# Performance work log

Hardware: AMD Instinct MI355X
Metric: run time of the kernel (lower is better)

## Reference

```python
import jax, jax.numpy as jnp
import numpy as np

PH, PW = 7, 7          # pooled output size (fixed by offset shape in module)
SPP = 2                # sample_per_part: bilinear samples per bin edge
SS = 0.0625            # spatial_scale = 1/16
TRANS_STD = 0.1


def setup_inputs() -> dict:
    key = jax.random.key(0)
    k1, k2, k3, k4, k5 = jax.random.split(key, 5)
    B, C, H, W = 8, 256, 168, 168
    N = 512
    img = W / SS  # input-image extent = 2688
    features = jax.random.normal(k1, (B, C, H, W), dtype=jnp.float32)
    bidx = jax.random.randint(k2, (N,), 0, B).astype(jnp.float32)
    xs = jnp.sort(jax.random.uniform(k3, (N, 2), minval=0.0, maxval=img - 1.0), axis=1)
    ys = jnp.sort(jax.random.uniform(k4, (N, 2), minval=0.0, maxval=img - 1.0), axis=1)
    rois = jnp.stack([bidx, xs[:, 0], ys[:, 0],
                      jnp.minimum(xs[:, 1] + 16.0, img - 1.0),
                      jnp.minimum(ys[:, 1] + 16.0, img - 1.0)], axis=1)
    offset = jax.random.normal(k5, (N, 2, PH, PW), dtype=jnp.float32)
    return {"features": features, "rois": rois, "offset": offset}


def _deform_roi_pool(features, rois, offset):
    B, C, H, W = features.shape
    off = offset * TRANS_STD  # module scales offsets by trans_std
    bidx = jax.lax.stop_gradient(rois[:, 0]).astype(jnp.int32)
    x1, y1, x2, y2 = rois[:, 1], rois[:, 2], rois[:, 3], rois[:, 4]
    # DCN kernel ROI geometry (0.5-pixel aligned, min size 0.1)
    sw = x1 * SS - 0.5
    sh = y1 * SS - 0.5
    rw = jnp.maximum((x2 + 1.0) * SS - 0.5 - sw, 0.1)
    rh = jnp.maximum((y2 + 1.0) * SS - 0.5 - sh, 0.1)
    bin_w, bin_h = rw / PW, rh / PH
    sub_w, sub_h = bin_w / SPP, bin_h / SPP

    e5 = lambda v: v[:, None, None, None, None]  # [N] -> [N,1,1,1,1]
    pw = jnp.arange(PW, dtype=features.dtype).reshape(1, 1, PW, 1, 1)
    ph = jnp.arange(PH, dtype=features.dtype).reshape(1, PH, 1, 1, 1)
    iw = (jnp.arange(SPP, dtype=features.dtype) + 0.5).reshape(1, 1, 1, 1, SPP)
    ih = (jnp.arange(SPP, dtype=features.dtype) + 0.5).reshape(1, 1, 1, SPP, 1)
    offx = off[:, 0][:, :, :, None, None]  # [N,PH,PW,1,1]
    offy = off[:, 1][:, :, :, None, None]

    # sample coords [N,PH,PW,SPP,SPP]: bin start + per-bin learned shift + sub-sample
    x = e5(sw) + pw * e5(bin_w) + offx * e5(rw) + iw * e5(sub_w)
    y = e5(sh) + ph * e5(bin_h) + offy * e5(rh) + ih * e5(sub_h)

    valid = (x > -0.5) & (x < W - 0.5) & (y > -0.5) & (y < H - 0.5)
    xc = jnp.clip(x, 0.0, W - 1.0)
    yc = jnp.clip(y, 0.0, H - 1.0)
    x0f, y0f = jnp.floor(xc), jnp.floor(yc)
    lx, ly = xc - x0f, yc - y0f
    x0 = x0f.astype(jnp.int32)
    y0 = y0f.astype(jnp.int32)
    x1i = jnp.minimum(x0 + 1, W - 1)
    y1i = jnp.minimum(y0 + 1, H - 1)

    # flat gather over (batch, h, w), channels vectorized
    featf = jnp.transpose(features, (0, 2, 3, 1)).reshape(B * H * W, C)
    base = e5(bidx) * (H * W)
    g = lambda yy, xx: featf[base + yy * W + xx]  # [N,PH,PW,SPP,SPP,C]

    w00 = ((1 - ly) * (1 - lx))[..., None]
    w01 = ((1 - ly) * lx)[..., None]
    w10 = (ly * (1 - lx))[..., None]
    w11 = (ly * lx)[..., None]
    val = w00 * g(y0, x0) + w01 * g(y0, x1i) + w10 * g(y1i, x0) + w11 * g(y1i, x1i)
    val = jnp.where(valid[..., None], val, 0.0)

    s = val.sum(axis=(3, 4))                                   # [N,PH,PW,C]
    cnt = valid.sum(axis=(3, 4)).astype(features.dtype)[..., None]
    out = jnp.where(cnt > 0, s / jnp.maximum(cnt, 1.0), 0.0)
    return jnp.transpose(out, (0, 3, 1, 2))                    # [N,C,PH,PW]


def reference(features, rois, offset):
    return _deform_roi_pool(features, rois, offset)
```

## Files before the change

### kernel.cpp

```cpp
#include <hip/hip_runtime.h>
#include <hip/hip_fp16.h>


#define PH_ 7
#define PW_ 7
#define SPP_ 2
#define SS_ 0.0625f
#define TRANS_STD_ 0.1f
#define B_ 8
#define C_ 256
#define H_ 168
#define W_ 168
#define N_ 512
#define HW_ (H_ * W_)
#define HW4_ (HW_ / 4)
#define BINS_ (PH_ * PW_)
#define NSUB_ (SPP_ * SPP_)
#define BLK_ 1024
#define RPC_ 20
#define PLN_ (HW_ + W_ + 4)

#define WS_LIST_OFF_   B_
#define WS_DESCA_OFF_I (B_ + B_ * N_)
#define DESCA_INTS_    (N_ * BINS_ * 4)
#define WS_DESCW_OFF_I (WS_DESCA_OFF_I + DESCA_INTS_)
#define DESCW_FLOATS_  (N_ * BINS_ * NSUB_ * 4)
#define WS_NEEDED_     ((size_t)(WS_DESCW_OFF_I + DESCW_FLOATS_) * 4)

__global__ __launch_bounds__(512) void build_roi_lists(
    const float* __restrict__ rois, int* __restrict__ ws)
{
    const int r = threadIdx.x;
    if (r < B_) ws[r] = 0;
    __syncthreads();
    const int b = (int)rois[r * 5 + 0];
    const int pos = atomicAdd(&ws[b], 1);
    ws[WS_LIST_OFF_ + b * N_ + pos] = r;
}

__global__ __launch_bounds__(64) void build_desc(
    const float* __restrict__ rois,
    const float* __restrict__ offset,
    int* __restrict__ ws)
{
    const int r   = blockIdx.x;
    const int bin = threadIdx.x;
    if (bin >= BINS_) return;
    const int ph = bin / PW_;
    const int pw = bin - ph * PW_;

    const float x1r = rois[r * 5 + 1];
    const float y1r = rois[r * 5 + 2];
    const float x2r = rois[r * 5 + 3];
    const float y2r = rois[r * 5 + 4];

    const float sw    = x1r * SS_ - 0.5f;
    const float sh    = y1r * SS_ - 0.5f;
    const float rw    = fmaxf((x2r + 1.0f) * SS_ - 0.5f - sw, 0.1f);
    const float rh    = fmaxf((y2r + 1.0f) * SS_ - 0.5f - sh, 0.1f);
    const float bin_w = rw * (1.0f / PW_);
    const float bin_h = rh * (1.0f / PH_);
    const float sub_w = bin_w * (1.0f / SPP_);
    const float sub_h = bin_h * (1.0f / SPP_);

    const float offx = offset[((r * 2 + 0) * PH_ + ph) * PW_ + pw] * TRANS_STD_;
    const float offy = offset[((r * 2 + 1) * PH_ + ph) * PW_ + pw] * TRANS_STD_;

    const float bx = sw + (float)pw * bin_w + offx * rw;
    const float by = sh + (float)ph * bin_h + offy * rh;

    unsigned idx[NSUB_];
    float w00[NSUB_], w01[NSUB_], w10[NSUB_], w11[NSUB_];
    int   vals[NSUB_];
    int   cnt = 0;
#pragma unroll
    for (int s = 0; s < NSUB_; ++s) {
        const int ihs = s >> 1;
        const int iws = s & 1;
        const float x = bx + ((float)iws + 0.5f) * sub_w;
        const float y = by + ((float)ihs + 0.5f) * sub_h;
        const int valid = (x > -0.5f) && (x < (float)W_ - 0.5f) &&
                          (y > -0.5f) && (y < (float)H_ - 0.5f);
        const float xc = fminf(fmaxf(x, 0.0f), (float)(W_ - 1));
        const float yc = fminf(fmaxf(y, 0.0f), (float)(H_ - 1));
        const float x0f = floorf(xc);
        const float y0f = floorf(yc);
        const int x0 = (int)x0f;
        const int y0 = (int)y0f;
        const float lx = xc - x0f;
        const float ly = yc - y0f;
        idx[s] = (unsigned)(y0 * W_ + x0);
        w00[s] = (1.0f - ly) * (1.0f - lx);
        w01[s] = (1.0f - ly) * lx;
        w10[s] = ly * (1.0f - lx);
        w11[s] = ly * lx;
        vals[s] = valid;
        cnt += valid;
    }
    const float inv = (cnt > 0) ? (1.0f / (float)cnt) : 0.0f;

    uint4*  descA = reinterpret_cast<uint4*> (ws + WS_DESCA_OFF_I);
    float4* descW = reinterpret_cast<float4*>(ws + WS_DESCW_OFF_I);

    const int rb = r * BINS_ + bin;
#pragma unroll
    for (int s = 0; s < NSUB_; ++s) {
        const float f = vals[s] ? inv : 0.0f;
        float4 w;
        w.x = w00[s] * f;
        w.y = w01[s] * f;
        w.z = w10[s] * f;
        w.w = w11[s] * f;
        descW[(size_t)rb * NSUB_ + s] = w;
    }
    uint4 a4;
    a4.x = idx[0]; a4.y = idx[1]; a4.z = idx[2]; a4.w = idx[3];
    descA[rb] = a4;
}

__global__ __launch_bounds__(BLK_, 8) void droi_pool_lds(
    const float* __restrict__ features,
    float* __restrict__ out,
    const int* __restrict__ ws)
{
    __shared__ __half plane[PLN_];

    const int c   = blockIdx.x;
    const int b   = blockIdx.y;
    const int tid = threadIdx.x;

    const float4* __restrict__ f4 =
        reinterpret_cast<const float4*>(features + (size_t)(b * C_ + c) * HW_);
    for (int i = tid; i < HW4_; i += BLK_) {
        const float4 v = f4[i];
        union { __half2 h[2]; float2 f2; } u;
        u.h[0].x = __float2half(v.x); u.h[0].y = __float2half(v.y);
        u.h[1].x = __float2half(v.z); u.h[1].y = __float2half(v.w);
        *reinterpret_cast<float2*>(&plane[i * 4]) = u.f2;
    }
    for (int i = HW_ + tid; i < PLN_; i += BLK_) plane[i] = __float2half(0.0f);
    __syncthreads();

    const int cnt_b = ws[b];
    const int* __restrict__ list = ws + WS_LIST_OFF_ + b * N_;
    const uint4* __restrict__ descA =
        reinterpret_cast<const uint4*>(ws + WS_DESCA_OFF_I);
    const float4* __restrict__ descW =
        reinterpret_cast<const float4*>(ws + WS_DESCW_OFF_I);

    const int q   = tid / BINS_;
    const int bin = tid - q * BINS_;
    const bool lane_ok = (q < RPC_);

    for (int base = 0; base < cnt_b; base += RPC_) {
        const int idx     = base + q;
        const bool active = lane_ok && (idx < cnt_b);
        const int r = list[active ? idx : 0];
        const int rb = r * BINS_ + bin;

        const uint4 a4 = descA[rb];
        const float4* __restrict__ wp = descW + (size_t)rb * NSUB_;
        const float4 w0 = wp[0];
        const float4 w1 = wp[1];
        const float4 w2 = wp[2];
        const float4 w3 = wp[3];

        float acc = 0.0f;
#define TAP(A, WV)                                                   \
        {                                                            \
            const int a = (int)(A);                                  \
            const float f00 = __half2float(plane[a]);                \
            const float f01 = __half2float(plane[a + 1]);            \
            const float f10 = __half2float(plane[a + W_]);           \
            const float f11 = __half2float(plane[a + W_ + 1]);       \
            acc += WV.x * f00 + WV.y * f01 + WV.z * f10 + WV.w * f11;\
        }
        TAP(a4.x, w0)
        TAP(a4.y, w1)
        TAP(a4.z, w2)
        TAP(a4.w, w3)
#undef TAP

        if (active) {
            out[((size_t)r * C_ + c) * BINS_ + bin] = acc;
        }
    }
}

__global__ __launch_bounds__(64) void droi_pool_fallback(
    const float* __restrict__ features,
    const float* __restrict__ rois,
    const float* __restrict__ offset,
    float* __restrict__ out)
{
    const int blk  = blockIdx.x;
    const int n    = blk >> 8;
    const int c    = blk & 255;
    const int lane = threadIdx.x;
    if (lane >= BINS_) return;
    const int ph = lane / PW_;
    const int pw = lane % PW_;

    const float r0  = rois[n * 5 + 0];
    const float x1r = rois[n * 5 + 1];
    const float y1r = rois[n * 5 + 2];
    const float x2r = rois[n * 5 + 3];
    const float y2r = rois[n * 5 + 4];
    const int   b   = (int)r0;

    const float sw    = x1r * SS_ - 0.5f;
    const float sh    = y1r * SS_ - 0.5f;
    const float rw    = fmaxf((x2r + 1.0f) * SS_ - 0.5f - sw, 0.1f);
    const float rh    = fmaxf((y2r + 1.0f) * SS_ - 0.5f - sh, 0.1f);
    const float bin_w = rw / PW_;
    const float bin_h = rh / PH_;
    const float sub_w = bin_w / SPP_;
    const float sub_h = bin_h / SPP_;

    const float offx = offset[((n * 2 + 0) * PH_ + ph) * PW_ + pw] * TRANS_STD_;
    const float offy = offset[((n * 2 + 1) * PH_ + ph) * PW_ + pw] * TRANS_STD_;

    const float bx = sw + (float)pw * bin_w + offx * rw;
    const float by = sh + (float)ph * bin_h + offy * rh;

    const float* __restrict__ f =
        features + (size_t)(b * C_ + c) * (size_t)HW_;

    float s = 0.0f;
    int cnt = 0;
#pragma unroll
    for (int ihs = 0; ihs < SPP_; ++ihs) {
#pragma unroll
        for (int iws = 0; iws < SPP_; ++iws) {
            const float x = bx + ((float)iws + 0.5f) * sub_w;
            const float y = by + ((float)ihs + 0.5f) * sub_h;
            const bool valid = (x > -0.5f) && (x < (float)W_ - 0.5f) &&
                               (y > -0.5f) && (y < (float)H_ - 0.5f);
            const float xc = fminf(fmaxf(x, 0.0f), (float)(W_ - 1));
            const float yc = fminf(fmaxf(y, 0.0f), (float)(H_ - 1));
            const float x0f = floorf(xc);
            const float y0f = floorf(yc);
            const float lx = xc - x0f;
            const float ly = yc - y0f;
            const int x0 = (int)x0f;
            const int y0 = (int)y0f;
            const int x1i = min(x0 + 1, W_ - 1);
            const int y1i = min(y0 + 1, H_ - 1);
            const float f00 = f[y0  * W_ + x0 ];
            const float f01 = f[y0  * W_ + x1i];
            const float f10 = f[y1i * W_ + x0 ];
            const float f11 = f[y1i * W_ + x1i];
            const float v = (1.0f - ly) * (1.0f - lx) * f00 +
                            (1.0f - ly) * lx          * f01 +
                            ly          * (1.0f - lx) * f10 +
                            ly          * lx          * f11;
            if (valid) { s += v; cnt += 1; }
        }
    }
    const float res = (cnt > 0) ? (s / (float)cnt) : 0.0f;
    out[(size_t)(n * C_ + c) * BINS_ + lane] = res;
}

extern "C" void kernel_launch(void* const* d_in, const int* in_sizes, int n_in,
                              void* d_out, int out_size, void* d_ws, size_t ws_size,
                              hipStream_t stream) {
    const float* features = (const float*)d_in[0];
    const float* rois     = (const float*)d_in[1];
    const float* offset   = (const float*)d_in[2];
    float*       out      = (float*)d_out;

    if (ws_size >= WS_NEEDED_) {
        int* ws = (int*)d_ws;
        hipLaunchKernelGGL(build_roi_lists, dim3(1), dim3(N_), 0, stream,
                           rois, ws);
        hipLaunchKernelGGL(build_desc, dim3(N_), dim3(64), 0, stream,
                           rois, offset, ws);
        hipLaunchKernelGGL(droi_pool_lds, dim3(C_, B_), dim3(BLK_), 0, stream,
                           features, out, ws);
    } else {
        hipLaunchKernelGGL(droi_pool_fallback, dim3(N_ * C_), dim3(64), 0, stream,
                           features, rois, offset, out);
    }
}
```

Measured before the change: 386.3 us.

## Process several channel planes per block with register-prefetched next plane

Each block now handles four channels instead of one. While it computes the bilinear samples for the current LDS plane, it loads the next channel's feature plane into registers, then converts and stores it to LDS after a barrier. The aim is to hide global-memory latency behind compute and to cut the number of blocks and repeated setup. The cost is 28 extra float4 registers per thread, which could limit occupancy at 1024 threads per block, and only 512 blocks launched.

```diff
diff --git a/kernel.cpp b/kernel.cpp
--- a/kernel.cpp
+++ b/kernel.cpp
@@ -19,6 +19,8 @@
 #define BLK_ 1024
 #define RPC_ 20
 #define PLN_ (HW_ + W_ + 4)
+#define PPB_ 4
+#define NLD_ 7
 
 #define WS_LIST_OFF_   B_
 #define WS_DESCA_OFF_I (B_ + B_ * N_)
@@ -118,6 +120,33 @@
     descA[rb] = a4;
 }
 
+
+#define LOAD_PLANE(cc)                                               \
+    do {                                                             \
+        const float4* __restrict__ f4 = fbase + (size_t)(cc) * HW4_; \
+        _Pragma("unroll")                                            \
+        for (int i = 0; i < NLD_; ++i) {                             \
+            const int ii = tid + i * BLK_;                           \
+            v[i] = f4[ii < HW4_ ? ii : 0];                           \
+        }                                                            \
+    } while (0)
+
+#define STORE_PLANE()                                                \
+    do {                                                             \
+        _Pragma("unroll")                                            \
+        for (int i = 0; i < NLD_; ++i) {                             \
+            const int ii = tid + i * BLK_;                           \
+            if (ii < HW4_) {                                         \
+                union { __half2 h[2]; float2 f2; } u;                \
+                u.h[0].x = __float2half(v[i].x);                     \
+                u.h[0].y = __float2half(v[i].y);                     \
+                u.h[1].x = __float2half(v[i].z);                     \
+                u.h[1].y = __float2half(v[i].w);                     \
+                *reinterpret_cast<float2*>(&plane[ii * 4]) = u.f2;   \
+            }                                                        \
+        }                                                            \
+    } while (0)
+
 __global__ __launch_bounds__(BLK_, 8) void droi_pool_lds(
     const float* __restrict__ features,
     float* __restrict__ out,
@@ -125,20 +154,18 @@
 {
     __shared__ __half plane[PLN_];
 
-    const int c   = blockIdx.x;
+    const int c0  = blockIdx.x * PPB_;
     const int b   = blockIdx.y;
     const int tid = threadIdx.x;
 
-    const float4* __restrict__ f4 =
-        reinterpret_cast<const float4*>(features + (size_t)(b * C_ + c) * HW_);
-    for (int i = tid; i < HW4_; i += BLK_) {
-        const float4 v = f4[i];
-        union { __half2 h[2]; float2 f2; } u;
-        u.h[0].x = __float2half(v.x); u.h[0].y = __float2half(v.y);
-        u.h[1].x = __float2half(v.z); u.h[1].y = __float2half(v.w);
-        *reinterpret_cast<float2*>(&plane[i * 4]) = u.f2;
-    }
+    const float4* __restrict__ fbase =
+        reinterpret_cast<const float4*>(features + (size_t)b * C_ * HW_);
+
+    float4 v[NLD_];
+
+    LOAD_PLANE(c0);
     for (int i = HW_ + tid; i < PLN_; i += BLK_) plane[i] = __float2half(0.0f);
+    STORE_PLANE();
     __syncthreads();
 
     const int cnt_b = ws[b];
@@ -152,38 +179,40 @@
     const int bin = tid - q * BINS_;
     const bool lane_ok = (q < RPC_);
 
-    for (int base = 0; base < cnt_b; base += RPC_) {
-        const int idx     = base + q;
-        const bool active = lane_ok && (idx < cnt_b);
-        const int r = list[active ? idx : 0];
-        const int rb = r * BINS_ + bin;
-
-        const uint4 a4 = descA[rb];
-        const float4* __restrict__ wp = descW + (size_t)rb * NSUB_;
-        const float4 w0 = wp[0];
-        const float4 w1 = wp[1];
-        const float4 w2 = wp[2];
-        const float4 w3 = wp[3];
-
-        float acc = 0.0f;
-#define TAP(A, WV)                                                   \
-        {                                                            \
-            const int a = (int)(A);                                  \
-            const float f00 = __half2float(plane[a]);                \
-            const float f01 = __half2float(plane[a + 1]);            \
-            const float f10 = __half2float(plane[a + W_]);           \
-            const float f11 = __half2float(plane[a + W_ + 1]);       \
-            acc += WV.x * f00 + WV.y * f01 + WV.z * f10 + WV.w * f11;\
+#pragma unroll
+    for (int p = 0; p < PPB_; ++p) {
+        const int c = c0 + p;
+
+        if (p + 1 < PPB_) LOAD_PLANE(c + 1);
+
+        for (int base = 0; base < cnt_b; base += RPC_) {
+            const int idx    = base + q;
+            const bool active = lane_ok && (idx < cnt_b);
+            if (active) {
+                const int r  = list[idx];
+                const int rb = r * BINS_ + bin;
+
+                const uint4 a4 = descA[rb];
+                const float4* __restrict__ wp = descW + (size_t)rb * NSUB_;
+
+                float acc = 0.0f;
+#pragma unroll
+                for (int s = 0; s < NSUB_; ++s) {
+                    const float4 w = wp[s];
+                    const int a = (int)((&a4.x)[s]);
+                    const float f00 = __half2float(plane[a]);
+                    const float f01 = __half2float(plane[a + 1]);
+                    const float f10 = __half2float(plane[a + W_]);
+                    const float f11 = __half2float(plane[a + W_ + 1]);
+                    acc += w.x * f00 + w.y * f01 + w.z * f10 + w.w * f11;
+                }
+                out[((size_t)r * C_ + c) * BINS_ + bin] = acc;
+            }
         }
-        TAP(a4.x, w0)
-        TAP(a4.y, w1)
-        TAP(a4.z, w2)
-        TAP(a4.w, w3)
-#undef TAP
-
-        if (active) {
-            out[((size_t)r * C_ + c) * BINS_ + bin] = acc;
-        }
+
+        __syncthreads();
+        if (p + 1 < PPB_) STORE_PLANE();
+        __syncthreads();
     }
 }
 
@@ -275,8 +304,8 @@
                            rois, ws);
         hipLaunchKernelGGL(build_desc, dim3(N_), dim3(64), 0, stream,
                            rois, offset, ws);
-        hipLaunchKernelGGL(droi_pool_lds, dim3(C_, B_), dim3(BLK_), 0, stream,
-                           features, out, ws);
+        hipLaunchKernelGGL(droi_pool_lds, dim3(C_ / PPB_, B_), dim3(BLK_),
+                           0, stream, features, out, ws);
     } else {
         hipLaunchKernelGGL(droi_pool_fallback, dim3(N_ * C_), dim3(64), 0, stream,
                            features, rois, offset, out);
```

After: 411.2 us. 1.06x slower.

## Warp-specialize pooling kernel with double-buffered LDS channel planes and merge setup kernels

Applied to the files above, without the earlier changes.

The pooling kernel now handles 8 channels per block. Half the threads act as producers: they convert the next channel plane to fp16 in a second LDS buffer while the other half gather bilinear taps from the current plane. The goal is to hide the global-load and convert phase behind the LDS gather work. The ROI-list build and descriptor build are also fused into one launch, removing a kernel launch. In exchange, the grid shrinks to 256 blocks and LDS use doubles, which likely allows only one block per CU. Only about 490 consumer threads compute taps, so gather throughput could drop.

```diff
diff --git a/kernel.cpp b/kernel.cpp
--- a/kernel.cpp
+++ b/kernel.cpp
@@ -17,8 +17,10 @@
 #define BINS_ (PH_ * PW_)
 #define NSUB_ (SPP_ * SPP_)
 #define BLK_ 1024
-#define RPC_ 20
 #define PLN_ (HW_ + W_ + 4)
+#define CPB_ 8
+#define NPROD_ 512
+#define CRPC_ 10
 
 #define WS_LIST_OFF_   B_
 #define WS_DESCA_OFF_I (B_ + B_ * N_)
@@ -27,24 +29,27 @@
 #define DESCW_FLOATS_  (N_ * BINS_ * NSUB_ * 4)
 #define WS_NEEDED_     ((size_t)(WS_DESCW_OFF_I + DESCW_FLOATS_) * 4)
 
-__global__ __launch_bounds__(512) void build_roi_lists(
-    const float* __restrict__ rois, int* __restrict__ ws)
-{
-    const int r = threadIdx.x;
-    if (r < B_) ws[r] = 0;
-    __syncthreads();
-    const int b = (int)rois[r * 5 + 0];
-    const int pos = atomicAdd(&ws[b], 1);
-    ws[WS_LIST_OFF_ + b * N_ + pos] = r;
-}
-
-__global__ __launch_bounds__(64) void build_desc(
+__global__ __launch_bounds__(64) void build_all(
     const float* __restrict__ rois,
     const float* __restrict__ offset,
     int* __restrict__ ws)
 {
-    const int r   = blockIdx.x;
-    const int bin = threadIdx.x;
+    const int blk = blockIdx.x;
+    const int t   = threadIdx.x;
+
+    if (blk == N_) {
+        if (t < B_) ws[t] = 0;
+        __syncthreads();
+        for (int r = t; r < N_; r += 64) {
+            const int b = (int)rois[r * 5 + 0];
+            const int pos = atomicAdd(&ws[b], 1);
+            ws[WS_LIST_OFF_ + b * N_ + pos] = r;
+        }
+        return;
+    }
+
+    const int r   = blk;
+    const int bin = t;
     if (bin >= BINS_) return;
     const int ph = bin / PW_;
     const int pw = bin - ph * PW_;
@@ -118,27 +123,34 @@
     descA[rb] = a4;
 }
 
-__global__ __launch_bounds__(BLK_, 8) void droi_pool_lds(
+__global__ __launch_bounds__(BLK_, 4) void droi_pool_pc(
     const float* __restrict__ features,
     float* __restrict__ out,
     const int* __restrict__ ws)
 {
-    __shared__ __half plane[PLN_];
-
-    const int c   = blockIdx.x;
+    __shared__ __half bufs[2][PLN_];
+
+    const int c0  = blockIdx.x * CPB_;
     const int b   = blockIdx.y;
     const int tid = threadIdx.x;
 
-    const float4* __restrict__ f4 =
-        reinterpret_cast<const float4*>(features + (size_t)(b * C_ + c) * HW_);
-    for (int i = tid; i < HW4_; i += BLK_) {
-        const float4 v = f4[i];
-        union { __half2 h[2]; float2 f2; } u;
-        u.h[0].x = __float2half(v.x); u.h[0].y = __float2half(v.y);
-        u.h[1].x = __float2half(v.z); u.h[1].y = __float2half(v.w);
-        *reinterpret_cast<float2*>(&plane[i * 4]) = u.f2;
-    }
-    for (int i = HW_ + tid; i < PLN_; i += BLK_) plane[i] = __float2half(0.0f);
+    const float4* __restrict__ fbase =
+        reinterpret_cast<const float4*>(features + (size_t)b * C_ * HW_);
+
+    for (int i = HW_ + tid; i < PLN_; i += BLK_) {
+        bufs[0][i] = __float2half(0.0f);
+        bufs[1][i] = __float2half(0.0f);
+    }
+    {
+        const float4* __restrict__ f4 = fbase + (size_t)c0 * HW4_;
+        for (int i = tid; i < HW4_; i += BLK_) {
+            const float4 v = f4[i];
+            union { __half2 h[2]; float2 f2; } u;
+            u.h[0].x = __float2half(v.x); u.h[0].y = __float2half(v.y);
+            u.h[1].x = __float2half(v.z); u.h[1].y = __float2half(v.w);
+            *reinterpret_cast<float2*>(&bufs[0][i * 4]) = u.f2;
+        }
+    }
     __syncthreads();
 
     const int cnt_b = ws[b];
@@ -148,42 +160,55 @@
     const float4* __restrict__ descW =
         reinterpret_cast<const float4*>(ws + WS_DESCW_OFF_I);
 
-    const int q   = tid / BINS_;
-    const int bin = tid - q * BINS_;
-    const bool lane_ok = (q < RPC_);
-
-    for (int base = 0; base < cnt_b; base += RPC_) {
-        const int idx     = base + q;
-        const bool active = lane_ok && (idx < cnt_b);
-        const int r = list[active ? idx : 0];
-        const int rb = r * BINS_ + bin;
-
-        const uint4 a4 = descA[rb];
-        const float4* __restrict__ wp = descW + (size_t)rb * NSUB_;
-        const float4 w0 = wp[0];
-        const float4 w1 = wp[1];
-        const float4 w2 = wp[2];
-        const float4 w3 = wp[3];
-
-        float acc = 0.0f;
-#define TAP(A, WV)                                                   \
-        {                                                            \
-            const int a = (int)(A);                                  \
-            const float f00 = __half2float(plane[a]);                \
-            const float f01 = __half2float(plane[a + 1]);            \
-            const float f10 = __half2float(plane[a + W_]);           \
-            const float f11 = __half2float(plane[a + W_ + 1]);       \
-            acc += WV.x * f00 + WV.y * f01 + WV.z * f10 + WV.w * f11;\
+    const bool consumer = (tid >= NPROD_);
+    const int  t   = tid - NPROD_;
+    const int  q   = consumer ? (t / BINS_) : 0;
+    const int  bin = consumer ? (t - q * BINS_) : 0;
+    const bool lane_ok = consumer && (q < CRPC_);
+
+    for (int p = 0; p < CPB_; ++p) {
+        const int c = c0 + p;
+        const __half* __restrict__ cur = bufs[p & 1];
+        __half*       __restrict__ nxt = bufs[(p & 1) ^ 1];
+
+        if (!consumer) {
+            if (p + 1 < CPB_) {
+                const float4* __restrict__ f4 = fbase + (size_t)(c + 1) * HW4_;
+                for (int i = tid; i < HW4_; i += NPROD_) {
+                    const float4 v = f4[i];
+                    union { __half2 h[2]; float2 f2; } u;
+                    u.h[0].x = __float2half(v.x); u.h[0].y = __float2half(v.y);
+                    u.h[1].x = __float2half(v.z); u.h[1].y = __float2half(v.w);
+                    *reinterpret_cast<float2*>(&nxt[i * 4]) = u.f2;
+                }
+            }
+        } else {
+            for (int base = 0; base < cnt_b; base += CRPC_) {
+                const int idx = base + q;
+                if (lane_ok && (idx < cnt_b)) {
+                    const int r  = list[idx];
+                    const int rb = r * BINS_ + bin;
+
+                    const uint4 a4 = descA[rb];
+                    const float4* __restrict__ wp = descW + (size_t)rb * NSUB_;
+
+                    float acc = 0.0f;
+#pragma unroll
+                    for (int s = 0; s < NSUB_; ++s) {
+                        const float4 w = wp[s];
+                        const int a = (int)((&a4.x)[s]);
+                        const float f00 = __half2float(cur[a]);
+                        const float f01 = __half2float(cur[a + 1]);
+                        const float f10 = __half2float(cur[a + W_]);
+                        const float f11 = __half2float(cur[a + W_ + 1]);
+                        acc += w.x * f00 + w.y * f01 + w.z * f10 + w.w * f11;
+                    }
+                    out[((size_t)r * C_ + c) * BINS_ + bin] = acc;
+                }
+            }
         }
-        TAP(a4.x, w0)
-        TAP(a4.y, w1)
-        TAP(a4.z, w2)
-        TAP(a4.w, w3)
-#undef TAP
-
-        if (active) {
-            out[((size_t)r * C_ + c) * BINS_ + bin] = acc;
-        }
+
+        __syncthreads();
     }
 }
 
@@ -271,12 +296,10 @@
 
     if (ws_size >= WS_NEEDED_) {
         int* ws = (int*)d_ws;
-        hipLaunchKernelGGL(build_roi_lists, dim3(1), dim3(N_), 0, stream,
-                           rois, ws);
-        hipLaunchKernelGGL(build_desc, dim3(N_), dim3(64), 0, stream,
+        hipLaunchKernelGGL(build_all, dim3(N_ + 1), dim3(64), 0, stream,
                            rois, offset, ws);
-        hipLaunchKernelGGL(droi_pool_lds, dim3(C_, B_), dim3(BLK_), 0, stream,
-                           features, out, ws);
+        hipLaunchKernelGGL(droi_pool_pc, dim3(C_ / CPB_, B_), dim3(BLK_),
+                           0, stream, features, out, ws);
     } else {
         hipLaunchKernelGGL(droi_pool_fallback, dim3(N_ * C_), dim3(64), 0, stream,
                            features, rois, offset, out);
```

Measured after the change: 381.6 us. No clear change (-1.2%).
